# Kernel optimization log

Hardware: AMD Instinct MI355X
Metric: run time of the kernel (lower is better)

Reference implementation:

```python
import jax, jax.numpy as jnp
import numpy as np

N = 10000          # num_nodes
E_DIR = 160000     # directed random edges before symmetrization
B = 8              # batch
IN = 64            # input_size per node
UNITS = 64         # num_units
K = 2              # max_diffusion_step -> num_matrices = K + 1
LAMBDA_MAX = 1.5   # stand-in for eigsh largest-eigenvalue estimate


def _build_scaled_laplacian():
    # L_scaled = (2/lambda_max) * (I - D^-1/2 A D^-1/2) - I, as sparse COO
    rng = np.random.default_rng(0)
    src = rng.integers(0, N, E_DIR)
    dst = rng.integers(0, N, E_DIR)
    # symmetrize A = max(A, A^T) by duplicating edges both ways
    r = np.concatenate([src, dst])
    c = np.concatenate([dst, src])
    w = np.ones(2 * E_DIR, np.float32)
    deg = np.zeros(N, np.float32)
    np.add.at(deg, r, w)
    d_inv_sqrt = np.where(deg > 0, deg ** -0.5, 0.0).astype(np.float32)
    coef = np.float32(2.0 / LAMBDA_MAX)
    off_vals = (-coef * d_inv_sqrt[r] * d_inv_sqrt[c] * w).astype(np.float32)
    diag_idx = np.arange(N, dtype=np.int32)
    diag_vals = np.full(N, coef - 1.0, np.float32)
    rows = np.concatenate([r.astype(np.int32), diag_idx])
    cols = np.concatenate([c.astype(np.int32), diag_idx])
    vals = np.concatenate([off_vals, diag_vals])
    return rows, cols, vals  # nnz = 2*E_DIR + N = 330000


def setup_inputs() -> dict:
    key = jax.random.key(0)
    k_in, k_w = jax.random.split(key)
    rows, cols, vals = _build_scaled_laplacian()
    num_matrices = K + 1
    fan_in = IN * num_matrices
    xavier = np.sqrt(6.0 / (fan_in + UNITS)).astype(np.float32)
    return {
        "inputs": jax.random.normal(k_in, (B, N * IN), dtype=jnp.float32),
        "rows": jnp.asarray(rows),
        "cols": jnp.asarray(cols),
        "vals": jnp.asarray(vals),
        "weights": jax.random.uniform(k_w, (fan_in, UNITS), dtype=jnp.float32,
                                      minval=-xavier, maxval=xavier),
        "biases": jnp.zeros((UNITS,), dtype=jnp.float32),
    }


def reference(inputs, rows, cols, vals, weights, biases):
    batch = inputs.shape[0]
    x = inputs.reshape(batch, N, -1)              # [B, N, in]
    in_size = x.shape[2]
    # x0: [N, in*B]
    x0 = jnp.transpose(x, (1, 2, 0)).reshape(N, in_size * batch)

    def spmm(h):  # sparse Laplacian @ dense
        return jax.ops.segment_sum(vals[:, None] * h[cols], rows, num_segments=N)

    # Chebyshev recursion: T0 = x0, T1 = L x0, Tk = 2 L Tk-1 - Tk-2
    xs = [x0]
    x1 = spmm(x0)
    xs.append(x1)
    xk_1, xk_2 = x1, x0
    for _ in range(2, K + 1):
        x2 = 2.0 * spmm(xk_1) - xk_2
        xs.append(x2)
        xk_1, xk_2 = x2, xk_1

    num_matrices = K + 1
    xcat = jnp.stack(xs, axis=0)                              # [M, N, in*B]
    xcat = xcat.reshape(num_matrices, N, in_size, batch)      # [M, N, in, B]
    xcat = jnp.transpose(xcat, (3, 1, 2, 0))                  # [B, N, in, M]
    xcat = xcat.reshape(batch * N, in_size * num_matrices)
    out = xcat @ weights + biases
    return out.reshape(batch, N, UNITS)
```

## Files before the change

### kernel.cpp

```cpp
#include <hip/hip_runtime.h>

#define N_NODES 10000
#define BATCH   8
#define IN_SZ   64
#define UNITS   64
#define ROW_U   256
#define ROW_U2  128
#define RCAP    96

typedef unsigned int uint;
typedef __attribute__((ext_vector_type(8))) short short8;
typedef __attribute__((ext_vector_type(4))) float float4v;
typedef __attribute__((ext_vector_type(2))) float float2v;
typedef __attribute__((ext_vector_type(2))) uint uint2v;

__device__ inline float bf_lo(uint u) { return __uint_as_float(u << 16); }
__device__ inline float bf_hi(uint u) { return __uint_as_float(u & 0xFFFF0000u); }
__device__ inline uint  f2bf_bits(float f) {
    uint u = __float_as_uint(f);
    uint r = ((u >> 16) & 1u) + 0x7FFFu;
    return (u + r) >> 16;
}
__device__ inline uint pack2(float a, float b) {
    return f2bf_bits(a) | (f2bf_bits(b) << 16);
}

__global__ __launch_bounds__(256) void k_transpose_scatter(
    const float2v* __restrict__ in2, uint* __restrict__ x0,
    const int* __restrict__ rows, const int* __restrict__ cols,
    const float* __restrict__ vals, int* __restrict__ cursor,
    uint2v* __restrict__ edges, int nnz) {
    int gid = blockIdx.x * 256 + threadIdx.x;
    if (gid < nnz) {
        int r   = rows[gid];
        int pos = r * RCAP + atomicAdd(&cursor[r], 1);
        uint2v ev;
        ev.x = (uint)cols[gid];
        ev.y = __float_as_uint(vals[gid]);
        edges[pos] = ev;
    }
    int n  = gid >> 8;
    int b  = (gid >> 5) & 7;
    int iu = gid & 31;
    float2v v = __builtin_nontemporal_load(&in2[(size_t)b * (N_NODES * 32) +
                                                (size_t)n * 32 + iu]);
    x0[gid] = pack2(v.x, v.y);
}

__global__ __launch_bounds__(256) void k_spmm(const int* __restrict__ cursor,
                                              const uint2v* __restrict__ edges,
                                              const uint2v* __restrict__ xin,
                                              uint2v* __restrict__ xout,
                                              const uint2v* __restrict__ xsub,
                                              float scale) {
    int wave = threadIdx.x >> 6;
    int lane = threadIdx.x & 63;
    int row  = blockIdx.x * 4 + wave;
    int col2 = blockIdx.y * 64 + lane;

    int start = row * RCAP;
    int cnt   = __builtin_amdgcn_readfirstlane(cursor[row]);
    int end   = start + ((cnt + 7) & ~7);

    float2v accA = {0.f, 0.f};
    float2v accB = {0.f, 0.f};

    for (int e = start; e < end; e += 8) {
        uint2v ev[8];
#pragma unroll
        for (int j = 0; j < 8; ++j) ev[j] = edges[e + j];
        uint2v x[8];
#pragma unroll
        for (int j = 0; j < 8; ++j)
            x[j] = xin[(size_t)ev[j].x * ROW_U2 + col2];
#pragma unroll
        for (int j = 0; j < 8; ++j) {
            float vj = __uint_as_float(ev[j].y);
            float2v vv = {vj, vj};
            float2v pA = {bf_lo(x[j].x), bf_hi(x[j].x)};
            float2v pB = {bf_lo(x[j].y), bf_hi(x[j].y)};
            accA += vv * pA;
            accB += vv * pB;
        }
    }

    float o0 = scale * accA.x, o1 = scale * accA.y;
    float o2 = scale * accB.x, o3 = scale * accB.y;
    if (xsub) {
        uint2v sx = __builtin_nontemporal_load(&xsub[(size_t)row * ROW_U2 + col2]);
        o0 -= bf_lo(sx.x); o1 -= bf_hi(sx.x);
        o2 -= bf_lo(sx.y); o3 -= bf_hi(sx.y);
    }
    uint2v o;
    o.x = pack2(o0, o1);
    o.y = pack2(o2, o3);
    __builtin_nontemporal_store(o, &xout[(size_t)row * ROW_U2 + col2]);
}

__global__ __launch_bounds__(256) void k_combine(const uint* __restrict__ x0,
                                                 const uint* __restrict__ x1,
                                                 const uint* __restrict__ x2,
                                                 const float* __restrict__ W,
                                                 const float* __restrict__ bias,
                                                 float* __restrict__ out) {
    __shared__ unsigned short sWt[64][200];
    int t = threadIdx.x;
    for (int e = t; e < 192 * 64; e += 256) {
        int f = e >> 6;
        int u = e & 63;
        int i = f / 3;
        int m = f - 3 * i;
        sWt[u][m * 64 + i] = (unsigned short)f2bf_bits(W[e]);
    }
    __syncthreads();

    int wave = t >> 6, lane = t & 63;
    int mrow = lane & 15, quad = lane >> 4;
    int n0   = blockIdx.x * 64 + wave * 16;
    int b    = blockIdx.y;

    const uint* xs[3] = {x0, x1, x2};
    int an = n0 + mrow;
    if (an > N_NODES - 1) an = N_NODES - 1;

    short8 af[6];
#pragma unroll
    for (int kb = 0; kb < 6; ++kb) {
        int mat = kb >> 1;
        af[kb] = __builtin_nontemporal_load(
            (const short8*)(xs[mat] + (size_t)an * ROW_U + b * 32 +
                            (kb & 1) * 16 + quad * 4));
    }

    float4v acc[4];
#pragma unroll
    for (int ut = 0; ut < 4; ++ut) acc[ut] = (float4v){0.f, 0.f, 0.f, 0.f};

#pragma unroll
    for (int kb = 0; kb < 6; ++kb)
#pragma unroll
        for (int ut = 0; ut < 4; ++ut)
            acc[ut] = __builtin_amdgcn_mfma_f32_16x16x32_bf16(
                af[kb],
                *(const short8*)&sWt[ut * 16 + mrow][kb * 32 + quad * 8],
                acc[ut], 0, 0, 0);

#pragma unroll
    for (int ut = 0; ut < 4; ++ut) {
        float bv = bias[ut * 16 + mrow];
        int u = ut * 16 + mrow;
#pragma unroll
        for (int r = 0; r < 4; ++r) {
            int n = n0 + quad * 4 + r;
            if (n < N_NODES)
                __builtin_nontemporal_store(acc[ut][r] + bv,
                    &out[((size_t)b * N_NODES + n) * UNITS + u]);
        }
    }
}

extern "C" void kernel_launch(void* const* d_in, const int* in_sizes, int n_in,
                              void* d_out, int out_size, void* d_ws, size_t ws_size,
                              hipStream_t stream) {
    const float* inputs = (const float*)d_in[0];
    const int*   rows   = (const int*)d_in[1];
    const int*   cols   = (const int*)d_in[2];
    const float* vals   = (const float*)d_in[3];
    const float* W      = (const float*)d_in[4];
    const float* bias   = (const float*)d_in[5];
    float*       out    = (float*)d_out;
    int nnz = in_sizes[1];

    char* p = (char*)d_ws;
    auto alloc = [&](size_t bytes) {
        char* r = p;
        p += (bytes + 255) & ~(size_t)255;
        return r;
    };
    uint*   x0      = (uint*)alloc(sizeof(uint) * (size_t)N_NODES * ROW_U);
    uint*   x1      = (uint*)alloc(sizeof(uint) * (size_t)N_NODES * ROW_U);
    uint*   x2      = (uint*)alloc(sizeof(uint) * (size_t)N_NODES * ROW_U);
    int*    cursor  = (int*)alloc(sizeof(int) * N_NODES);
    uint2v* edges   = (uint2v*)alloc(sizeof(uint2v) * (size_t)N_NODES * RCAP);
    size_t  zspan   = (char*)(edges + (size_t)N_NODES * RCAP) - (char*)cursor;

    (void)hipMemsetAsync(cursor, 0, zspan, stream);
    k_transpose_scatter<<<N_NODES, 256, 0, stream>>>((const float2v*)inputs, x0,
                                                     rows, cols, vals, cursor,
                                                     edges, nnz);
    dim3 sgrid(N_NODES / 4, 2);
    k_spmm<<<sgrid, 256, 0, stream>>>(cursor, edges, (const uint2v*)x0,
                                      (uint2v*)x1, nullptr, 1.0f);
    k_spmm<<<sgrid, 256, 0, stream>>>(cursor, edges, (const uint2v*)x1,
                                      (uint2v*)x2, (const uint2v*)x0, 2.0f);
    dim3 cgrid((N_NODES + 63) / 64, BATCH);
    k_combine<<<cgrid, 256, 0, stream>>>(x0, x1, x2, W, bias, out);
}
```

Baseline: 198.5 us.

## Split feature rows into four column quarters and stop zeroing edge buffer

Intermediate Chebyshev buffers are re-laid out as four contiguous column quarters, each 64 uints per node, so each SpMM block gathers 256-byte rows from a 2.5 MB slab that fits in cache better. The SpMM grid doubles in y and each lane handles one uint instead of two. The memset now clears only the cursor array, not the whole 7.7 MB edge buffer, and the leftover edges are handled with a masked tail whose column index is sanitised because those slots hold uninitialised data. The trade-off is twice as many edge-list reads and four times as many gather requests, though each request is narrower.

Result: no change. 195.7 us (-1.4%).

```diff
diff --git a/kernel.cpp b/kernel.cpp
--- a/kernel.cpp
+++ b/kernel.cpp
@@ -5,8 +5,8 @@
 #define IN_SZ   64
 #define UNITS   64
 #define ROW_U   256
-#define ROW_U2  128
 #define RCAP    96
+#define STR     (N_NODES * 64)
 
 typedef unsigned int uint;
 typedef __attribute__((ext_vector_type(8))) short short8;
@@ -44,57 +44,75 @@
     int iu = gid & 31;
     float2v v = __builtin_nontemporal_load(&in2[(size_t)b * (N_NODES * 32) +
                                                 (size_t)n * 32 + iu]);
-    x0[gid] = pack2(v.x, v.y);
+    int q = (gid >> 6) & 3;
+    x0[(size_t)q * STR + (size_t)n * 64 + (gid & 63)] = pack2(v.x, v.y);
 }
 
 __global__ __launch_bounds__(256) void k_spmm(const int* __restrict__ cursor,
                                               const uint2v* __restrict__ edges,
-                                              const uint2v* __restrict__ xin,
-                                              uint2v* __restrict__ xout,
-                                              const uint2v* __restrict__ xsub,
+                                              const uint* __restrict__ xin,
+                                              uint* __restrict__ xout,
+                                              const uint* __restrict__ xsub,
                                               float scale) {
     int wave = threadIdx.x >> 6;
     int lane = threadIdx.x & 63;
     int row  = blockIdx.x * 4 + wave;
-    int col2 = blockIdx.y * 64 + lane;
-
-    int start = row * RCAP;
-    int cnt   = __builtin_amdgcn_readfirstlane(cursor[row]);
-    int end   = start + ((cnt + 7) & ~7);
-
-    float2v accA = {0.f, 0.f};
-    float2v accB = {0.f, 0.f};
-
-    for (int e = start; e < end; e += 8) {
+    int q    = blockIdx.y;
+
+    const uint* xq = xin + (size_t)q * STR;
+    int base = row * RCAP;
+    int cnt  = __builtin_amdgcn_readfirstlane(cursor[row]);
+
+    float2v acc = {0.f, 0.f};
+
+    int full_end = base + (cnt & ~7);
+    for (int e = base; e < full_end; e += 8) {
         uint2v ev[8];
 #pragma unroll
         for (int j = 0; j < 8; ++j) ev[j] = edges[e + j];
-        uint2v x[8];
+        uint x[8];
 #pragma unroll
         for (int j = 0; j < 8; ++j)
-            x[j] = xin[(size_t)ev[j].x * ROW_U2 + col2];
+            x[j] = xq[(size_t)ev[j].x * 64 + lane];
 #pragma unroll
         for (int j = 0; j < 8; ++j) {
             float vj = __uint_as_float(ev[j].y);
             float2v vv = {vj, vj};
-            float2v pA = {bf_lo(x[j].x), bf_hi(x[j].x)};
-            float2v pB = {bf_lo(x[j].y), bf_hi(x[j].y)};
-            accA += vv * pA;
-            accB += vv * pB;
-        }
-    }
-
-    float o0 = scale * accA.x, o1 = scale * accA.y;
-    float o2 = scale * accB.x, o3 = scale * accB.y;
+            float2v pp = {bf_lo(x[j]), bf_hi(x[j])};
+            acc += vv * pp;
+        }
+    }
+    int rem = cnt & 7;
+    if (rem) {
+        int e = full_end;
+        uint2v ev[8];
+#pragma unroll
+        for (int j = 0; j < 8; ++j) ev[j] = edges[e + j];
+        uint x[8];
+#pragma unroll
+        for (int j = 0; j < 8; ++j) {
+            uint c = ev[j].x & 16383u;
+            if (c >= N_NODES) c = 0;
+            x[j] = xq[(size_t)c * 64 + lane];
+        }
+#pragma unroll
+        for (int j = 0; j < 8; ++j) {
+            float vj = (j < rem) ? __uint_as_float(ev[j].y) : 0.f;
+            float2v vv = {vj, vj};
+            float2v pp = {bf_lo(x[j]), bf_hi(x[j])};
+            acc += vv * pp;
+        }
+    }
+
+    float o0 = scale * acc.x, o1 = scale * acc.y;
     if (xsub) {
-        uint2v sx = __builtin_nontemporal_load(&xsub[(size_t)row * ROW_U2 + col2]);
-        o0 -= bf_lo(sx.x); o1 -= bf_hi(sx.x);
-        o2 -= bf_lo(sx.y); o3 -= bf_hi(sx.y);
-    }
-    uint2v o;
-    o.x = pack2(o0, o1);
-    o.y = pack2(o2, o3);
-    __builtin_nontemporal_store(o, &xout[(size_t)row * ROW_U2 + col2]);
+        uint sx = __builtin_nontemporal_load(
+            &xsub[(size_t)q * STR + (size_t)row * 64 + lane]);
+        o0 -= bf_lo(sx);
+        o1 -= bf_hi(sx);
+    }
+    __builtin_nontemporal_store(pack2(o0, o1),
+        &xout[(size_t)q * STR + (size_t)row * 64 + lane]);
 }
 
 __global__ __launch_bounds__(256) void k_combine(const uint* __restrict__ x0,
@@ -127,9 +145,11 @@
 #pragma unroll
     for (int kb = 0; kb < 6; ++kb) {
         int mat = kb >> 1;
+        int c_u = b * 32 + (kb & 1) * 16 + quad * 4;
+        int q   = c_u >> 6;
         af[kb] = __builtin_nontemporal_load(
-            (const short8*)(xs[mat] + (size_t)an * ROW_U + b * 32 +
-                            (kb & 1) * 16 + quad * 4));
+            (const short8*)(xs[mat] + (size_t)q * STR + (size_t)an * 64 +
+                            (c_u & 63)));
     }
 
     float4v acc[4];
@@ -177,22 +197,19 @@
         p += (bytes + 255) & ~(size_t)255;
         return r;
     };
-    uint*   x0      = (uint*)alloc(sizeof(uint) * (size_t)N_NODES * ROW_U);
-    uint*   x1      = (uint*)alloc(sizeof(uint) * (size_t)N_NODES * ROW_U);
-    uint*   x2      = (uint*)alloc(sizeof(uint) * (size_t)N_NODES * ROW_U);
-    int*    cursor  = (int*)alloc(sizeof(int) * N_NODES);
-    uint2v* edges   = (uint2v*)alloc(sizeof(uint2v) * (size_t)N_NODES * RCAP);
-    size_t  zspan   = (char*)(edges + (size_t)N_NODES * RCAP) - (char*)cursor;
-
-    (void)hipMemsetAsync(cursor, 0, zspan, stream);
+    uint*   x0     = (uint*)alloc(sizeof(uint) * (size_t)N_NODES * ROW_U);
+    uint*   x1     = (uint*)alloc(sizeof(uint) * (size_t)N_NODES * ROW_U);
+    uint*   x2     = (uint*)alloc(sizeof(uint) * (size_t)N_NODES * ROW_U);
+    int*    cursor = (int*)alloc(sizeof(int) * N_NODES);
+    uint2v* edges  = (uint2v*)alloc(sizeof(uint2v) * (size_t)N_NODES * RCAP);
+
+    (void)hipMemsetAsync(cursor, 0, sizeof(int) * N_NODES, stream);
     k_transpose_scatter<<<N_NODES, 256, 0, stream>>>((const float2v*)inputs, x0,
                                                      rows, cols, vals, cursor,
                                                      edges, nnz);
-    dim3 sgrid(N_NODES / 4, 2);
-    k_spmm<<<sgrid, 256, 0, stream>>>(cursor, edges, (const uint2v*)x0,
-                                      (uint2v*)x1, nullptr, 1.0f);
-    k_spmm<<<sgrid, 256, 0, stream>>>(cursor, edges, (const uint2v*)x1,
-                                      (uint2v*)x2, (const uint2v*)x0, 2.0f);
+    dim3 sgrid(N_NODES / 4, 4);
+    k_spmm<<<sgrid, 256, 0, stream>>>(cursor, edges, x0, x1, nullptr, 1.0f);
+    k_spmm<<<sgrid, 256, 0, stream>>>(cursor, edges, x1, x2, x0, 2.0f);
     dim3 cgrid((N_NODES + 63) / 64, BATCH);
     k_combine<<<cgrid, 256, 0, stream>>>(x0, x1, x2, W, bias, out);
 }
```
